# Kernel optimization log

Measured on AMD Instinct MI355X. Metric: run time of the kernel, lower is better.

Reference implementation:

```python
import jax, jax.numpy as jnp
import numpy as np


def setup_inputs() -> dict:
    key = jax.random.key(0)
    kq, kk, kv = jax.random.split(key, 3)
    B, H, S, D = 2, 16, 2048, 64
    Q = jax.random.normal(kq, (B, H, S, D), dtype=jnp.float32)
    K = jax.random.normal(kk, (B, H, S, D), dtype=jnp.float32)
    V = jax.random.normal(kv, (B, H, S, D), dtype=jnp.float32)
    return {"Q": Q, "K": K, "V": V}


def reference(Q, K, V):
    # Faithful to the torch module: NO 1/sqrt(d_k) scaling (d_k is computed
    # but never used in the original forward).
    scores = jnp.einsum('bhqd,bhkd->bhqk', Q, K)      # [B,H,S,S]
    attn = jax.nn.softmax(scores, axis=-1)
    out = jnp.einsum('bhqk,bhkd->bhqd', attn, V)      # [B,H,S,D]
    return out
```

## Files before the change

### kernel.cpp

```cpp
#include <hip/hip_runtime.h>


typedef __bf16    bf16_t;
typedef _Float16  f16_t;
typedef __bf16    bf16x8 __attribute__((ext_vector_type(8)));
typedef _Float16  f16x8  __attribute__((ext_vector_type(8)));
typedef float     f32x4  __attribute__((ext_vector_type(4)));

constexpr int S  = 2048;
constexpr int Dh = 64;
constexpr int KT = 64;

__device__ __forceinline__ int sw(int row, int col) {
    return row * 64 + ((((col >> 3) ^ (row & 7)) << 3) | (col & 7));
}

__global__ __launch_bounds__(256, 4)
void attn_kernel(const float* __restrict__ Qg,
                 const float* __restrict__ Kg,
                 const float* __restrict__ Vg,
                 float* __restrict__ Og)
{
    __shared__ f16_t  Khs[KT * Dh];
    __shared__ bf16_t Vts[Dh * KT];
    __shared__ bf16_t Pbs[64 * KT];

    const int tid  = threadIdx.x;
    const int lane = tid & 63;
    const int wv   = tid >> 6;
    const int l15  = lane & 15;
    const int qd   = lane >> 4;
    const int wb   = wv * 16;

    const int head = blockIdx.x >> 5;
    const int qt   = blockIdx.x & 31;

    const float* Qp = Qg + ((size_t)head * S + (size_t)qt * 64) * Dh;
    const float* Kp = Kg + (size_t)head * S * Dh;
    const float* Vp = Vg + (size_t)head * S * Dh;
    float*       Op = Og + ((size_t)head * S + (size_t)qt * 64) * Dh;

    const int skey = tid >> 4;
    const int sc4  = (tid & 15) * 4;
    const int vkb  = (tid >> 4) * 4;
    const int vc4  = (tid & 15) * 4;

    f16x8 qf[2];
    {
        const float* qrow = Qp + (size_t)(wb + l15) * Dh;
        #pragma unroll
        for (int ks = 0; ks < 2; ++ks) {
            const float* p = qrow + ks * 32 + qd * 8;
            const float4 a = *(const float4*)(p);
            const float4 b = *(const float4*)(p + 4);
            const float xs[8] = {a.x, a.y, a.z, a.w, b.x, b.y, b.z, b.w};
            #pragma unroll
            for (int j = 0; j < 8; ++j) qf[ks][j] = (f16_t)xs[j];
        }
    }

    f32x4 oa[4];
    float lp[4];
    #pragma unroll
    for (int t = 0; t < 4; ++t) {
        oa[t] = (f32x4){0.f, 0.f, 0.f, 0.f};
        lp[t] = 0.f;
    }

    float4 kbuf[4], vbuf[4];
    {
        const float* Kc = Kp;
        const float* Vc = Vp;
        #pragma unroll
        for (int it = 0; it < 4; ++it)
            kbuf[it] = *(const float4*)(Kc + (size_t)(it * 16 + skey) * Dh + sc4);
        #pragma unroll
        for (int i = 0; i < 4; ++i)
            vbuf[i] = *(const float4*)(Vc + (size_t)(vkb + i) * Dh + vc4);
    }

    #pragma unroll 1
    for (int ch = 0; ch < S / KT; ++ch) {
        __syncthreads();

        #pragma unroll
        for (int it = 0; it < 4; ++it) {
            const float xs[4] = {kbuf[it].x, kbuf[it].y, kbuf[it].z, kbuf[it].w};
            union { f16_t h[4]; uint2 u; } ph;
            #pragma unroll
            for (int j = 0; j < 4; ++j) ph.h[j] = (f16_t)xs[j];
            *(uint2*)&Khs[sw(it * 16 + skey, sc4)] = ph.u;
        }
        {
            const float rs[4][4] = {{vbuf[0].x, vbuf[1].x, vbuf[2].x, vbuf[3].x},
                                    {vbuf[0].y, vbuf[1].y, vbuf[2].y, vbuf[3].y},
                                    {vbuf[0].z, vbuf[1].z, vbuf[2].z, vbuf[3].z},
                                    {vbuf[0].w, vbuf[1].w, vbuf[2].w, vbuf[3].w}};
            #pragma unroll
            for (int i = 0; i < 4; ++i) {
                union { bf16_t h[4]; uint2 u; } pv;
                #pragma unroll
                for (int j = 0; j < 4; ++j) pv.h[j] = (bf16_t)rs[i][j];
                *(uint2*)&Vts[sw(vc4 + i, vkb)] = pv.u;
            }
        }
        __syncthreads();

        if (ch + 1 < S / KT) {
            const float* Kc = Kp + (size_t)(ch + 1) * KT * Dh;
            const float* Vc = Vp + (size_t)(ch + 1) * KT * Dh;
            #pragma unroll
            for (int it = 0; it < 4; ++it)
                kbuf[it] = *(const float4*)(Kc + (size_t)(it * 16 + skey) * Dh + sc4);
            #pragma unroll
            for (int i = 0; i < 4; ++i)
                vbuf[i] = *(const float4*)(Vc + (size_t)(vkb + i) * Dh + vc4);
        }

        f32x4 sc[4];
        #pragma unroll
        for (int nt = 0; nt < 4; ++nt) sc[nt] = (f32x4){0.f, 0.f, 0.f, 0.f};
        #pragma unroll
        for (int ks = 0; ks < 2; ++ks) {
            const int co = ks * 32 + qd * 8;
            #pragma unroll
            for (int nt = 0; nt < 4; ++nt) {
                const f16x8 bk = *(const f16x8*)&Khs[sw(nt * 16 + l15, co)];
                sc[nt] = __builtin_amdgcn_mfma_f32_16x16x32_f16(qf[ks], bk, sc[nt], 0, 0, 0);
            }
        }

        #pragma unroll
        for (int nt = 0; nt < 4; ++nt) {
            #pragma unroll
            for (int r = 0; r < 4; ++r) {
                const int row = wb + qd * 4 + r;
                const bf16_t b = (bf16_t)__expf(sc[nt][r]);
                lp[r] += (float)b;
                Pbs[sw(row, nt * 16 + l15)] = b;
            }
        }

        #pragma unroll
        for (int ks = 0; ks < 2; ++ks) {
            const int co = ks * 32 + qd * 8;
            const bf16x8 pa = *(const bf16x8*)&Pbs[sw(wb + l15, co)];
            #pragma unroll
            for (int dt = 0; dt < 4; ++dt) {
                const bf16x8 vb = *(const bf16x8*)&Vts[sw(dt * 16 + l15, co)];
                oa[dt] = __builtin_amdgcn_mfma_f32_16x16x32_bf16(pa, vb, oa[dt], 0, 0, 0);
            }
        }
    }

    float inv[4];
    #pragma unroll
    for (int r = 0; r < 4; ++r) {
        float v = lp[r];
        #pragma unroll
        for (int m = 1; m <= 8; m <<= 1) v += __shfl_xor(v, m, 64);
        inv[r] = 1.0f / v;
    }

    #pragma unroll
    for (int dt = 0; dt < 4; ++dt) {
        #pragma unroll
        for (int r = 0; r < 4; ++r) {
            const int row = wb + qd * 4 + r;
            Op[(size_t)row * Dh + dt * 16 + l15] = oa[dt][r] * inv[r];
        }
    }
}

extern "C" void kernel_launch(void* const* d_in, const int* in_sizes, int n_in,
                              void* d_out, int out_size, void* d_ws, size_t ws_size,
                              hipStream_t stream)
{
    const float* Q = (const float*)d_in[0];
    const float* K = (const float*)d_in[1];
    const float* V = (const float*)d_in[2];
    float*       O = (float*)d_out;

    dim3 grid(32 * 32);
    dim3 block(256);
    attn_kernel<<<grid, block, 0, stream>>>(Q, K, V, O);
}
```

Before: 162.5 us.

## Use 128-row query tiles with split-KV partials and a combine kernel

Each block now covers 128 query rows (two 16-row subtiles per wave), so every staged K/V chunk is reused across twice as many queries. To keep the grid at 1024 blocks, the key range is split into two halves that write unnormalized partial outputs and row sums to workspace, and a second kernel sums and normalizes them. The QK^T MFMA is transposed (K as the A operand) so P can be stored as packed 4-element writes. The cost is an extra launch plus a round trip of partials through global memory, and more registers per wave at the same launch bounds; the old single-pass path remains as a fallback when workspace is too small.

```diff
diff --git a/kernel.cpp b/kernel.cpp
--- a/kernel.cpp
+++ b/kernel.cpp
@@ -10,44 +10,54 @@
 constexpr int S  = 2048;
 constexpr int Dh = 64;
 constexpr int KT = 64;
+constexpr int QT = 128;
 
 __device__ __forceinline__ int sw(int row, int col) {
     return row * 64 + ((((col >> 3) ^ (row & 7)) << 3) | (col & 7));
 }
 
+template<bool SPLIT>
 __global__ __launch_bounds__(256, 4)
 void attn_kernel(const float* __restrict__ Qg,
                  const float* __restrict__ Kg,
                  const float* __restrict__ Vg,
-                 float* __restrict__ Og)
+                 float* __restrict__ Og,
+                 float* __restrict__ Opart,
+                 float* __restrict__ lpart)
 {
     __shared__ f16_t  Khs[KT * Dh];
     __shared__ bf16_t Vts[Dh * KT];
-    __shared__ bf16_t Pbs[64 * KT];
+    __shared__ bf16_t Pbs[QT * Dh];
 
     const int tid  = threadIdx.x;
     const int lane = tid & 63;
     const int wv   = tid >> 6;
     const int l15  = lane & 15;
     const int qd   = lane >> 4;
-    const int wb   = wv * 16;
-
-    const int head = blockIdx.x >> 5;
-    const int qt   = blockIdx.x & 31;
-
-    const float* Qp = Qg + ((size_t)head * S + (size_t)qt * 64) * Dh;
+    const int wb   = wv * 32;
+
+    const int bx   = blockIdx.x;
+    const int head = bx & 31;
+    const int r5   = bx >> 5;
+    const int qt   = SPLIT ? (r5 >> 1) : r5;
+    const int half = SPLIT ? (r5 & 1) : 0;
+    const int tile = head * 16 + qt;
+    const int ch0  = SPLIT ? half * 16 : 0;
+    const int nch  = SPLIT ? 16 : 32;
+
+    const float* Qp = Qg + (size_t)tile * QT * Dh;
     const float* Kp = Kg + (size_t)head * S * Dh;
     const float* Vp = Vg + (size_t)head * S * Dh;
-    float*       Op = Og + ((size_t)head * S + (size_t)qt * 64) * Dh;
 
     const int skey = tid >> 4;
     const int sc4  = (tid & 15) * 4;
     const int vkb  = (tid >> 4) * 4;
     const int vc4  = (tid & 15) * 4;
 
-    f16x8 qf[2];
-    {
-        const float* qrow = Qp + (size_t)(wb + l15) * Dh;
+    f16x8 qf[2][2];
+    #pragma unroll
+    for (int sub = 0; sub < 2; ++sub) {
+        const float* qrow = Qp + (size_t)(wb + sub * 16 + l15) * Dh;
         #pragma unroll
         for (int ks = 0; ks < 2; ++ks) {
             const float* p = qrow + ks * 32 + qd * 8;
@@ -55,22 +65,23 @@
             const float4 b = *(const float4*)(p + 4);
             const float xs[8] = {a.x, a.y, a.z, a.w, b.x, b.y, b.z, b.w};
             #pragma unroll
-            for (int j = 0; j < 8; ++j) qf[ks][j] = (f16_t)xs[j];
-        }
-    }
-
-    f32x4 oa[4];
-    float lp[4];
+            for (int j = 0; j < 8; ++j) qf[sub][ks][j] = (f16_t)xs[j];
+        }
+    }
+
+    f32x4 oa[2][4];
+    float lp[2];
     #pragma unroll
-    for (int t = 0; t < 4; ++t) {
-        oa[t] = (f32x4){0.f, 0.f, 0.f, 0.f};
-        lp[t] = 0.f;
+    for (int s2 = 0; s2 < 2; ++s2) {
+        lp[s2] = 0.f;
+        #pragma unroll
+        for (int t = 0; t < 4; ++t) oa[s2][t] = (f32x4){0.f, 0.f, 0.f, 0.f};
     }
 
     float4 kbuf[4], vbuf[4];
     {
-        const float* Kc = Kp;
-        const float* Vc = Vp;
+        const float* Kc = Kp + (size_t)ch0 * KT * Dh;
+        const float* Vc = Vp + (size_t)ch0 * KT * Dh;
         #pragma unroll
         for (int it = 0; it < 4; ++it)
             kbuf[it] = *(const float4*)(Kc + (size_t)(it * 16 + skey) * Dh + sc4);
@@ -80,7 +91,7 @@
     }
 
     #pragma unroll 1
-    for (int ch = 0; ch < S / KT; ++ch) {
+    for (int ci = 0; ci < nch; ++ci) {
         __syncthreads();
 
         #pragma unroll
@@ -106,9 +117,9 @@
         }
         __syncthreads();
 
-        if (ch + 1 < S / KT) {
-            const float* Kc = Kp + (size_t)(ch + 1) * KT * Dh;
-            const float* Vc = Vp + (size_t)(ch + 1) * KT * Dh;
+        if (ci + 1 < nch) {
+            const float* Kc = Kp + (size_t)(ch0 + ci + 1) * KT * Dh;
+            const float* Vc = Vp + (size_t)(ch0 + ci + 1) * KT * Dh;
             #pragma unroll
             for (int it = 0; it < 4; ++it)
                 kbuf[it] = *(const float4*)(Kc + (size_t)(it * 16 + skey) * Dh + sc4);
@@ -117,59 +128,109 @@
                 vbuf[i] = *(const float4*)(Vc + (size_t)(vkb + i) * Dh + vc4);
         }
 
-        f32x4 sc[4];
-        #pragma unroll
-        for (int nt = 0; nt < 4; ++nt) sc[nt] = (f32x4){0.f, 0.f, 0.f, 0.f};
+        #pragma unroll
+        for (int np = 0; np < 2; ++np) {
+            f32x4 st[2][2];
+            #pragma unroll
+            for (int s2 = 0; s2 < 2; ++s2)
+                #pragma unroll
+                for (int t = 0; t < 2; ++t) st[s2][t] = (f32x4){0.f, 0.f, 0.f, 0.f};
+            #pragma unroll
+            for (int ks = 0; ks < 2; ++ks) {
+                const int co = ks * 32 + qd * 8;
+                const f16x8 ak0 = *(const f16x8*)&Khs[sw((np * 2 + 0) * 16 + l15, co)];
+                const f16x8 ak1 = *(const f16x8*)&Khs[sw((np * 2 + 1) * 16 + l15, co)];
+                #pragma unroll
+                for (int s2 = 0; s2 < 2; ++s2) {
+                    st[s2][0] = __builtin_amdgcn_mfma_f32_16x16x32_f16(ak0, qf[s2][ks], st[s2][0], 0, 0, 0);
+                    st[s2][1] = __builtin_amdgcn_mfma_f32_16x16x32_f16(ak1, qf[s2][ks], st[s2][1], 0, 0, 0);
+                }
+            }
+            #pragma unroll
+            for (int s2 = 0; s2 < 2; ++s2) {
+                #pragma unroll
+                for (int t = 0; t < 2; ++t) {
+                    union { bf16_t h[4]; uint2 u; } pb;
+                    #pragma unroll
+                    for (int r = 0; r < 4; ++r) {
+                        const bf16_t b = (bf16_t)__expf(st[s2][t][r]);
+                        lp[s2] += (float)b;
+                        pb.h[r] = b;
+                    }
+                    *(uint2*)&Pbs[sw(wb + s2 * 16 + l15, (np * 2 + t) * 16 + qd * 4)] = pb.u;
+                }
+            }
+        }
+
         #pragma unroll
         for (int ks = 0; ks < 2; ++ks) {
             const int co = ks * 32 + qd * 8;
-            #pragma unroll
-            for (int nt = 0; nt < 4; ++nt) {
-                const f16x8 bk = *(const f16x8*)&Khs[sw(nt * 16 + l15, co)];
-                sc[nt] = __builtin_amdgcn_mfma_f32_16x16x32_f16(qf[ks], bk, sc[nt], 0, 0, 0);
-            }
-        }
-
-        #pragma unroll
-        for (int nt = 0; nt < 4; ++nt) {
-            #pragma unroll
-            for (int r = 0; r < 4; ++r) {
-                const int row = wb + qd * 4 + r;
-                const bf16_t b = (bf16_t)__expf(sc[nt][r]);
-                lp[r] += (float)b;
-                Pbs[sw(row, nt * 16 + l15)] = b;
-            }
-        }
-
-        #pragma unroll
-        for (int ks = 0; ks < 2; ++ks) {
-            const int co = ks * 32 + qd * 8;
-            const bf16x8 pa = *(const bf16x8*)&Pbs[sw(wb + l15, co)];
+            const bf16x8 pa0 = *(const bf16x8*)&Pbs[sw(wb + l15,      co)];
+            const bf16x8 pa1 = *(const bf16x8*)&Pbs[sw(wb + 16 + l15, co)];
             #pragma unroll
             for (int dt = 0; dt < 4; ++dt) {
                 const bf16x8 vb = *(const bf16x8*)&Vts[sw(dt * 16 + l15, co)];
-                oa[dt] = __builtin_amdgcn_mfma_f32_16x16x32_bf16(pa, vb, oa[dt], 0, 0, 0);
-            }
-        }
-    }
-
-    float inv[4];
+                oa[0][dt] = __builtin_amdgcn_mfma_f32_16x16x32_bf16(pa0, vb, oa[0][dt], 0, 0, 0);
+                oa[1][dt] = __builtin_amdgcn_mfma_f32_16x16x32_bf16(pa1, vb, oa[1][dt], 0, 0, 0);
+            }
+        }
+    }
+
     #pragma unroll
-    for (int r = 0; r < 4; ++r) {
-        float v = lp[r];
-        #pragma unroll
-        for (int m = 1; m <= 8; m <<= 1) v += __shfl_xor(v, m, 64);
-        inv[r] = 1.0f / v;
-    }
-
-    #pragma unroll
-    for (int dt = 0; dt < 4; ++dt) {
-        #pragma unroll
-        for (int r = 0; r < 4; ++r) {
-            const int row = wb + qd * 4 + r;
-            Op[(size_t)row * Dh + dt * 16 + l15] = oa[dt][r] * inv[r];
-        }
-    }
+    for (int s2 = 0; s2 < 2; ++s2) {
+        lp[s2] += __shfl_xor(lp[s2], 16, 64);
+        lp[s2] += __shfl_xor(lp[s2], 32, 64);
+    }
+
+    if (SPLIT) {
+        float* Po = Opart + (size_t)(tile * 2 + half) * (QT * Dh);
+        float* lq = lpart + (size_t)(tile * 2 + half) * QT;
+        #pragma unroll
+        for (int s2 = 0; s2 < 2; ++s2) {
+            if (qd == 0) lq[wb + s2 * 16 + l15] = lp[s2];
+            #pragma unroll
+            for (int r = 0; r < 4; ++r) {
+                const int row = wb + s2 * 16 + qd * 4 + r;
+                #pragma unroll
+                for (int dt = 0; dt < 4; ++dt)
+                    Po[(size_t)row * Dh + dt * 16 + l15] = oa[s2][dt][r];
+            }
+        }
+    } else {
+        float* Op = Og + (size_t)tile * QT * Dh;
+        #pragma unroll
+        for (int s2 = 0; s2 < 2; ++s2) {
+            #pragma unroll
+            for (int r = 0; r < 4; ++r) {
+                const float inv = 1.0f / __shfl(lp[s2], qd * 4 + r, 64);
+                const int row = wb + s2 * 16 + qd * 4 + r;
+                #pragma unroll
+                for (int dt = 0; dt < 4; ++dt)
+                    Op[(size_t)row * Dh + dt * 16 + l15] = oa[s2][dt][r] * inv;
+            }
+        }
+    }
+}
+
+__global__ __launch_bounds__(256)
+void combine_kernel(const float* __restrict__ Opart,
+                    const float* __restrict__ lpart,
+                    float* __restrict__ Og)
+{
+    const int i  = blockIdx.x * 256 + threadIdx.x;
+    const int q  = i >> 11;
+    const int rw = (i >> 4) & 127;
+    const size_t e = (size_t)(i & 2047) * 4;
+    const float4 a = *(const float4*)(Opart + (size_t)(2 * q)     * (QT * Dh) + e);
+    const float4 b = *(const float4*)(Opart + (size_t)(2 * q + 1) * (QT * Dh) + e);
+    const float  l = lpart[(size_t)(2 * q) * QT + rw] + lpart[(size_t)(2 * q + 1) * QT + rw];
+    const float inv = 1.0f / l;
+    float4 o;
+    o.x = (a.x + b.x) * inv;
+    o.y = (a.y + b.y) * inv;
+    o.z = (a.z + b.z) * inv;
+    o.w = (a.w + b.w) * inv;
+    *(float4*)(Og + (size_t)i * 4) = o;
 }
 
 extern "C" void kernel_launch(void* const* d_in, const int* in_sizes, int n_in,
@@ -181,7 +242,20 @@
     const float* V = (const float*)d_in[2];
     float*       O = (float*)d_out;
 
-    dim3 grid(32 * 32);
-    dim3 block(256);
-    attn_kernel<<<grid, block, 0, stream>>>(Q, K, V, O);
-}
+    constexpr size_t NPART       = 1024;
+    constexpr size_t OPART_ELEMS = NPART * QT * Dh;
+    constexpr size_t LPART_ELEMS = NPART * QT;
+    constexpr size_t NEED = (OPART_ELEMS + LPART_ELEMS) * sizeof(float);
+
+    if (ws_size >= NEED) {
+        float* Opart = (float*)d_ws;
+        float* lpart = Opart + OPART_ELEMS;
+        attn_kernel<true><<<dim3(1024), dim3(256), 0, stream>>>(
+            Q, K, V, nullptr, Opart, lpart);
+        const int n4 = (int)(OPART_ELEMS / 2 / 4);
+        combine_kernel<<<dim3(n4 / 256), dim3(256), 0, stream>>>(Opart, lpart, O);
+    } else {
+        attn_kernel<false><<<dim3(512), dim3(256), 0, stream>>>(
+            Q, K, V, O, nullptr, nullptr);
+    }
+}
```

Result: faster. 153.5 us (-5.6%).
